# Optimization experiments

Measured on AMD Instinct MI355X. Metric: run time of the kernel, lower is better.

The kernel has to match this reference:

```python
import jax, jax.numpy as jnp
import numpy as np

N_NODES = 100000
N_EDGES = 1600000
D_IN = 128
D_OUT = 128
K_HOPS = 2


def gcn_norm(edge_index, num_nodes):
    # Add self-loops (weight 1), compute symmetric normalization
    # norm_e = deg^{-1/2}[src] * deg^{-1/2}[dst], deg over destination index.
    loop = jnp.arange(num_nodes, dtype=edge_index.dtype)
    src = jnp.concatenate([edge_index[0], loop])
    dst = jnp.concatenate([edge_index[1], loop])
    w = jnp.ones(src.shape[0], dtype=jnp.float32)
    deg = jax.ops.segment_sum(w, dst, num_segments=num_nodes)
    dinv = jnp.where(deg > 0, jax.lax.rsqrt(deg), 0.0)
    norm = dinv[src] * dinv[dst]
    return src, dst, norm


def setup_inputs() -> dict:
    key = jax.random.key(0)
    k1, k2, k3, k4 = jax.random.split(key, 4)
    x = jax.random.normal(k1, (N_NODES, D_IN), dtype=jnp.float32)
    edge_index = jax.random.randint(k2, (2, N_EDGES), 0, N_NODES, dtype=jnp.int64)
    # SGConv linear params (Glorot-ish scale)
    W = jax.random.normal(k3, (D_IN, D_OUT), dtype=jnp.float32) / np.sqrt(D_IN)
    b = jnp.zeros((D_OUT,), dtype=jnp.float32)
    return {"x": x, "edge_index": edge_index, "W": W, "b": b}


def reference(x, edge_index, W, b):
    n = x.shape[0]
    src, dst, norm = gcn_norm(edge_index, n)
    h = x
    for _ in range(K_HOPS):
        # gather source features, scale by edge norm, scatter-add to destinations
        h = jax.ops.segment_sum(h[src] * norm[:, None], dst, num_segments=n)
    return h @ W + b
```

## Files before the change

kernel.cpp:

```cpp
#include <hip/hip_runtime.h>
#include <hip/hip_bf16.h>


#define DFEAT 128
#define ELLW 64
#define ABLK 4096
#define CAP 4608
#define NBUCKMAX 512

typedef __attribute__((ext_vector_type(8))) short short8;
typedef __attribute__((ext_vector_type(4))) float f32x4;
typedef __attribute__((ext_vector_type(4))) unsigned int u32x4;

__device__ __forceinline__ float bf2f(unsigned short u) {
    union { unsigned int i; float f; } t;
    t.i = ((unsigned int)u) << 16;
    return t.f;
}

__device__ __forceinline__ unsigned short f2bf(float f) {
    union { float f; unsigned int i; } t;
    t.f = f;
    unsigned int lsb = (t.i >> 16) & 1u;
    t.i += 0x7fffu + lsb;
    return (unsigned short)(t.i >> 16);
}

__device__ __forceinline__ void accum8(float* acc, uint4 u, float w) {
    acc[0] += bf2f((unsigned short)(u.x & 0xffffu)) * w;
    acc[1] += bf2f((unsigned short)(u.x >> 16)) * w;
    acc[2] += bf2f((unsigned short)(u.y & 0xffffu)) * w;
    acc[3] += bf2f((unsigned short)(u.y >> 16)) * w;
    acc[4] += bf2f((unsigned short)(u.z & 0xffffu)) * w;
    acc[5] += bf2f((unsigned short)(u.z >> 16)) * w;
    acc[6] += bf2f((unsigned short)(u.w & 0xffffu)) * w;
    acc[7] += bf2f((unsigned short)(u.w >> 16)) * w;
}

__global__ void k_detect(const unsigned short* __restrict__ xs,
                         const int* __restrict__ ei, int* __restrict__ flags,
                         int* __restrict__ bucketCnt) {
    __shared__ int s_f32, s_oddnz;
    if (threadIdx.x == 0) { s_f32 = 0; s_oddnz = 0; }
    for (int t = threadIdx.x; t < NBUCKMAX; t += 256) bucketCnt[t] = 0;
    __syncthreads();
    int bad = 0;
    for (int i = threadIdx.x; i < 16384; i += 256) {
        unsigned int e = (xs[i] >> 7) & 0xFFu;
        if (e >= 0xC0u) bad = 1;
    }
    if (bad) atomicOr(&s_f32, 1);
    int oddnz = 0;
    for (int i = threadIdx.x; i < 4096; i += 256) {
        if (ei[2 * i + 1] != 0) oddnz = 1;
    }
    if (oddnz) atomicOr(&s_oddnz, 1);
    __syncthreads();
    if (threadIdx.x == 0) {
        flags[0] = s_f32;
        flags[1] = s_oddnz ? 0 : 1;
    }
}

__global__ void k_prepB(const void* __restrict__ Wraw, const int* __restrict__ flags,
                        unsigned short* __restrict__ Bf) {
    int t = blockIdx.x * 256 + threadIdx.x;
    if (t >= 2048) return;
    int lane = t & 63;
    int chunk = (t >> 6) & 3;
    int ntile = t >> 8;
    int ncol = ntile * 16 + (lane & 15);
    int k0 = chunk * 32 + (lane >> 4) * 8;
    int isf = flags[0];
    const float* Wf = (const float*)Wraw;
    const unsigned short* Wb = (const unsigned short*)Wraw;
    unsigned short* o = Bf + (size_t)t * 8;
#pragma unroll
    for (int j = 0; j < 8; j++) {
        int idx = (k0 + j) * DFEAT + ncol;
        o[j] = isf ? f2bf(Wf[idx]) : Wb[idx];
    }
}

__global__ __launch_bounds__(256) void k_bucketA(const int* __restrict__ ei, int E, int n,
                                                 const int* __restrict__ flags,
                                                 int* __restrict__ bucketCnt,
                                                 unsigned int* __restrict__ buck) {
    __shared__ int hist[NBUCKMAX];
    __shared__ int base[NBUCKMAX];
    for (int t = threadIdx.x; t < NBUCKMAX; t += 256) hist[t] = 0;
    __syncthreads();
    int e0 = blockIdx.x * ABLK;
    int e1 = min(E, e0 + ABLK);
    int i64 = flags[1];
    for (int e = e0 + (int)threadIdx.x; e < e1; e += 256) {
        int d = i64 ? ei[2 * (E + e)] : ei[E + e];
        atomicAdd(&hist[d >> 8], 1);
    }
    __syncthreads();
    for (int t = threadIdx.x; t < NBUCKMAX; t += 256) {
        int c = hist[t];
        base[t] = c ? atomicAdd(bucketCnt + t, c) : 0;
        hist[t] = 0;
    }
    __syncthreads();
    for (int e = e0 + (int)threadIdx.x; e < e1; e += 256) {
        int d = i64 ? ei[2 * (E + e)] : ei[E + e];
        int s = i64 ? ei[2 * e] : ei[e];
        int b = d >> 8;
        int pos = base[b] + atomicAdd(&hist[b], 1);
        if (pos < CAP)
            buck[(size_t)b * CAP + pos] = (unsigned int)s | ((unsigned int)(d & 255) << 17);
    }
}

__global__ __launch_bounds__(256) void k_bucketB(const unsigned int* __restrict__ buck,
                                                 const int* __restrict__ bucketCnt, int n,
                                                 int* __restrict__ cnt,
                                                 int* __restrict__ ell) {
    __shared__ int lcnt[256];
    int b = blockIdx.x;
    lcnt[threadIdx.x] = 0;
    __syncthreads();
    int m = min(bucketCnt[b], CAP);
    int node0 = b << 8;
    const unsigned int* bp = buck + (size_t)b * CAP;
    for (int i = threadIdx.x; i < m; i += 256) {
        unsigned int w = __builtin_nontemporal_load(bp + i);
        int s = (int)(w & 0x1FFFFu);
        int dl = (int)(w >> 17);
        int pos = atomicAdd(&lcnt[dl], 1);
        if (pos < ELLW) ell[(size_t)(node0 + dl) * ELLW + pos] = s;
    }
    __syncthreads();
    int node = node0 + (int)threadIdx.x;
    if (node < n) cnt[node] = lcnt[threadIdx.x];
}

__global__ __launch_bounds__(256) void k_gemm0(const void* __restrict__ xraw,
                                               const unsigned short* __restrict__ Bf,
                                               const int* __restrict__ flags,
                                               unsigned short* __restrict__ h0, int n) {
    __shared__ unsigned short thi[16 * 136];
    __shared__ unsigned short tlo[16 * 136];
    int wave = threadIdx.x >> 6;
    int lane = threadIdx.x & 63;
    int g = lane >> 4, c = lane & 15;
    int trow = wave * 4 + g;
    int node = blockIdx.x * 16 + trow;
    int isf = flags[0];

    uint4 ohi = {0, 0, 0, 0}, olo = {0, 0, 0, 0};
    if (node < n) {
        if (isf) {
            const float* xf = (const float*)xraw;
            f32x4 v0 = __builtin_nontemporal_load((const f32x4*)(xf + (size_t)node * DFEAT + c * 8));
            f32x4 v1 = __builtin_nontemporal_load((const f32x4*)(xf + (size_t)node * DFEAT + c * 8 + 4));
            float vv[8] = {v0[0], v0[1], v0[2], v0[3], v1[0], v1[1], v1[2], v1[3]};
            unsigned short h[8], l[8];
#pragma unroll
            for (int j = 0; j < 8; j++) {
                h[j] = f2bf(vv[j]);
                l[j] = f2bf(vv[j] - bf2f(h[j]));
            }
            ohi.x = (unsigned int)h[0] | ((unsigned int)h[1] << 16);
            ohi.y = (unsigned int)h[2] | ((unsigned int)h[3] << 16);
            ohi.z = (unsigned int)h[4] | ((unsigned int)h[5] << 16);
            ohi.w = (unsigned int)h[6] | ((unsigned int)h[7] << 16);
            olo.x = (unsigned int)l[0] | ((unsigned int)l[1] << 16);
            olo.y = (unsigned int)l[2] | ((unsigned int)l[3] << 16);
            olo.z = (unsigned int)l[4] | ((unsigned int)l[5] << 16);
            olo.w = (unsigned int)l[6] | ((unsigned int)l[7] << 16);
        } else {
            u32x4 u = __builtin_nontemporal_load(
                (const u32x4*)((const unsigned short*)xraw + (size_t)node * DFEAT + c * 8));
            ohi.x = u[0]; ohi.y = u[1]; ohi.z = u[2]; ohi.w = u[3];
        }
    }
    *(uint4*)(thi + trow * 136 + c * 8) = ohi;
    *(uint4*)(tlo + trow * 136 + c * 8) = olo;
    __syncthreads();

    int m = c, quad = g;
    f32x4 acc2[2];
    acc2[0] = (f32x4){0.f, 0.f, 0.f, 0.f};
    acc2[1] = (f32x4){0.f, 0.f, 0.f, 0.f};
#pragma unroll
    for (int c2 = 0; c2 < 4; c2++) {
        short8 ah = *(const short8*)(thi + m * 136 + c2 * 32 + quad * 8);
        short8 al = *(const short8*)(tlo + m * 136 + c2 * 32 + quad * 8);
#pragma unroll
        for (int t = 0; t < 2; t++) {
            int nt = wave * 2 + t;
            short8 bfr = *(const short8*)(Bf + ((size_t)(nt * 4 + c2) * 64 + lane) * 8);
            acc2[t] = __builtin_amdgcn_mfma_f32_16x16x32_bf16(ah, bfr, acc2[t], 0, 0, 0);
            acc2[t] = __builtin_amdgcn_mfma_f32_16x16x32_bf16(al, bfr, acc2[t], 0, 0, 0);
        }
    }

#pragma unroll
    for (int t = 0; t < 2; t++) {
        int col = (wave * 2 + t) * 16 + m;
#pragma unroll
        for (int r2 = 0; r2 < 4; r2++) {
            int grow = blockIdx.x * 16 + quad * 4 + r2;
            if (grow < n)
                __builtin_nontemporal_store(f2bf(acc2[t][r2]), h0 + (size_t)grow * DFEAT + col);
        }
    }
}

__device__ __forceinline__ void hop_accum(const unsigned short* __restrict__ fb,
                                          const int* __restrict__ ell,
                                          const int* __restrict__ cnt,
                                          int node, int lane, float* acc) {
    int g = lane >> 4, c = lane & 15;
    int deg = min(cnt[node], ELLW);
    const int* row = ell + (size_t)node * ELLW;
    float wd = rsqrtf((float)(cnt[node] + 1));
#pragma unroll
    for (int j = 0; j < 8; j++) acc[j] = 0.f;

    if (g == 0) {
        uint4 u = *(const uint4*)(fb + (size_t)node * DFEAT + c * 8);
        accum8(acc, u, wd * wd);
    }
    int last = deg - 1;
    for (int base = 0; base < deg; base += 16) {
        int k0 = base + g, k1 = k0 + 4, k2 = k0 + 8, k3 = k0 + 12;
        int s0 = __builtin_nontemporal_load(row + min(k0, last));
        int s1 = __builtin_nontemporal_load(row + min(k1, last));
        int s2 = __builtin_nontemporal_load(row + min(k2, last));
        int s3 = __builtin_nontemporal_load(row + min(k3, last));
        uint4 u0 = *(const uint4*)(fb + (size_t)s0 * DFEAT + c * 8);
        uint4 u1 = *(const uint4*)(fb + (size_t)s1 * DFEAT + c * 8);
        uint4 u2 = *(const uint4*)(fb + (size_t)s2 * DFEAT + c * 8);
        uint4 u3 = *(const uint4*)(fb + (size_t)s3 * DFEAT + c * 8);
        float w0 = (k0 < deg) ? rsqrtf((float)(cnt[s0] + 1)) * wd : 0.f;
        float w1 = (k1 < deg) ? rsqrtf((float)(cnt[s1] + 1)) * wd : 0.f;
        float w2 = (k2 < deg) ? rsqrtf((float)(cnt[s2] + 1)) * wd : 0.f;
        float w3 = (k3 < deg) ? rsqrtf((float)(cnt[s3] + 1)) * wd : 0.f;
        accum8(acc, u0, w0);
        accum8(acc, u1, w1);
        accum8(acc, u2, w2);
        accum8(acc, u3, w3);
    }
#pragma unroll
    for (int j = 0; j < 8; j++) {
        acc[j] += __shfl_xor(acc[j], 16);
        acc[j] += __shfl_xor(acc[j], 32);
    }
}

__global__ __launch_bounds__(256) void k_hop(const unsigned short* __restrict__ src,
                                             const int* __restrict__ ell,
                                             const int* __restrict__ cnt,
                                             unsigned short* __restrict__ outb, int n) {
    int node = blockIdx.x * 4 + (threadIdx.x >> 6);
    if (node >= n) return;
    int lane = threadIdx.x & 63;
    int g = lane >> 4, c = lane & 15;
    float acc[8];
    hop_accum(src, ell, cnt, node, lane, acc);
    if (g == 0) {
        uint4 o;
        o.x = (unsigned int)f2bf(acc[0]) | ((unsigned int)f2bf(acc[1]) << 16);
        o.y = (unsigned int)f2bf(acc[2]) | ((unsigned int)f2bf(acc[3]) << 16);
        o.z = (unsigned int)f2bf(acc[4]) | ((unsigned int)f2bf(acc[5]) << 16);
        o.w = (unsigned int)f2bf(acc[6]) | ((unsigned int)f2bf(acc[7]) << 16);
        *(uint4*)(outb + (size_t)node * DFEAT + c * 8) = o;
    }
}

__global__ __launch_bounds__(256) void k_hop2_out(const unsigned short* __restrict__ src,
                                                  const int* __restrict__ ell,
                                                  const int* __restrict__ cnt,
                                                  const void* __restrict__ braw,
                                                  const int* __restrict__ flags,
                                                  void* __restrict__ outraw, int n) {
    int node = blockIdx.x * 4 + (threadIdx.x >> 6);
    if (node >= n) return;
    int lane = threadIdx.x & 63;
    int g = lane >> 4, c = lane & 15;
    float acc[8];
    hop_accum(src, ell, cnt, node, lane, acc);
    if (g == 0) {
        int isf = flags[0];
        const float* bf32 = (const float*)braw;
        const unsigned short* bb16 = (const unsigned short*)braw;
#pragma unroll
        for (int j = 0; j < 8; j++)
            acc[j] += isf ? bf32[c * 8 + j] : bf2f(bb16[c * 8 + j]);
        if (isf) {
            float* outf = (float*)outraw;
            *(float4*)(outf + (size_t)node * DFEAT + c * 8) =
                (float4){acc[0], acc[1], acc[2], acc[3]};
            *(float4*)(outf + (size_t)node * DFEAT + c * 8 + 4) =
                (float4){acc[4], acc[5], acc[6], acc[7]};
        } else {
            unsigned short* outb = (unsigned short*)outraw;
            uint4 o;
            o.x = (unsigned int)f2bf(acc[0]) | ((unsigned int)f2bf(acc[1]) << 16);
            o.y = (unsigned int)f2bf(acc[2]) | ((unsigned int)f2bf(acc[3]) << 16);
            o.z = (unsigned int)f2bf(acc[4]) | ((unsigned int)f2bf(acc[5]) << 16);
            o.w = (unsigned int)f2bf(acc[6]) | ((unsigned int)f2bf(acc[7]) << 16);
            *(uint4*)(outb + (size_t)node * DFEAT + c * 8) = o;
        }
    }
}

extern "C" void kernel_launch(void* const* d_in, const int* in_sizes, int n_in,
                              void* d_out, int out_size, void* d_ws, size_t ws_size,
                              hipStream_t stream) {
    const void* x = d_in[0];
    const int* ei = (const int*)d_in[1];
    const void* W = d_in[2];
    const void* b = d_in[3];

    const int n = in_sizes[0] / DFEAT;
    const int E = in_sizes[1] / 2;

    int* ell = (int*)d_ws;
    unsigned short* h1 = (unsigned short*)(ell + (size_t)n * ELLW);
    int* cnt = (int*)(h1 + (size_t)n * DFEAT);
    int* flags = cnt + n;
    int* bucketCnt = flags + 4;
    unsigned short* Bf = (unsigned short*)(bucketCnt + NBUCKMAX);
    unsigned short* h0 = (unsigned short*)d_out;
    unsigned int* buck = (unsigned int*)((char*)d_out + (size_t)out_size
                                         - (size_t)NBUCKMAX * CAP * 4);

    k_detect<<<1, 256, 0, stream>>>((const unsigned short*)x, ei, flags, bucketCnt);

    k_prepB<<<8, 256, 0, stream>>>(W, flags, Bf);

    int nbuck = (n + 255) >> 8;
    int ablocks = (E + ABLK - 1) / ABLK;
    k_bucketA<<<ablocks, 256, 0, stream>>>(ei, E, n, flags, bucketCnt, buck);
    k_bucketB<<<nbuck, 256, 0, stream>>>(buck, bucketCnt, n, cnt, ell);

    k_gemm0<<<(n + 15) / 16, 256, 0, stream>>>(x, Bf, flags, h0, n);

    k_hop<<<(n + 3) / 4, 256, 0, stream>>>(h0, ell, cnt, h1, n);

    k_hop2_out<<<(n + 3) / 4, 256, 0, stream>>>(h1, ell, cnt, b, flags, d_out, n);
}
```

Measured before the change: 350.7 us.

## Fold GCN degree normalization into node features, drop per-edge weights

Factors the symmetric norm so node features are pre-scaled by deg^-1/2 (in the GEMM epilogue and between hops), letting the hop loops do plain unweighted sums with no per-edge cnt gathers or rsqrt. ELL rows are padded with self-indices to multiples of 16, and a correction weight on the self term makes the padding cancel, so the gather loop needs no bounds clamps. The bucketing kernel caches destination indices in shared memory and staggers global atomics, and detection now runs across 8 blocks after a memset. The change adds extra per-node scaling steps and bf16 rounding of the pre-scaled values, which may shift accuracy slightly.

```diff
diff --git a/kernel.cpp b/kernel.cpp
--- a/kernel.cpp
+++ b/kernel.cpp
@@ -11,6 +11,7 @@
 typedef __attribute__((ext_vector_type(8))) short short8;
 typedef __attribute__((ext_vector_type(4))) float f32x4;
 typedef __attribute__((ext_vector_type(4))) unsigned int u32x4;
+typedef __attribute__((ext_vector_type(4))) int i32x4;
 
 __device__ __forceinline__ float bf2f(unsigned short u) {
     union { unsigned int i; float f; } t;
@@ -37,29 +38,32 @@
     acc[7] += bf2f((unsigned short)(u.w >> 16)) * w;
 }
 
+__device__ __forceinline__ void add8(float* acc, uint4 u) {
+    union { unsigned int i; float f; } a;
+    a.i = u.x << 16;          acc[0] += a.f;
+    a.i = u.x & 0xffff0000u;  acc[1] += a.f;
+    a.i = u.y << 16;          acc[2] += a.f;
+    a.i = u.y & 0xffff0000u;  acc[3] += a.f;
+    a.i = u.z << 16;          acc[4] += a.f;
+    a.i = u.z & 0xffff0000u;  acc[5] += a.f;
+    a.i = u.w << 16;          acc[6] += a.f;
+    a.i = u.w & 0xffff0000u;  acc[7] += a.f;
+}
+
 __global__ void k_detect(const unsigned short* __restrict__ xs,
-                         const int* __restrict__ ei, int* __restrict__ flags,
-                         int* __restrict__ bucketCnt) {
-    __shared__ int s_f32, s_oddnz;
-    if (threadIdx.x == 0) { s_f32 = 0; s_oddnz = 0; }
-    for (int t = threadIdx.x; t < NBUCKMAX; t += 256) bucketCnt[t] = 0;
-    __syncthreads();
+                         const int* __restrict__ ei, int* __restrict__ flags) {
+    int t = blockIdx.x * 256 + (int)threadIdx.x;
     int bad = 0;
-    for (int i = threadIdx.x; i < 16384; i += 256) {
+    for (int i = t; i < 16384; i += 2048) {
         unsigned int e = (xs[i] >> 7) & 0xFFu;
         if (e >= 0xC0u) bad = 1;
     }
-    if (bad) atomicOr(&s_f32, 1);
+    if (__any(bad) && (threadIdx.x & 63) == 0) atomicOr(flags, 1);
     int oddnz = 0;
-    for (int i = threadIdx.x; i < 4096; i += 256) {
+    for (int i = t; i < 4096; i += 2048) {
         if (ei[2 * i + 1] != 0) oddnz = 1;
     }
-    if (oddnz) atomicOr(&s_oddnz, 1);
-    __syncthreads();
-    if (threadIdx.x == 0) {
-        flags[0] = s_f32;
-        flags[1] = s_oddnz ? 0 : 1;
-    }
+    if (__any(oddnz) && (threadIdx.x & 63) == 0) atomicOr(flags + 1, 1);
 }
 
 __global__ void k_prepB(const void* __restrict__ Wraw, const int* __restrict__ flags,
@@ -86,29 +90,35 @@
                                                  const int* __restrict__ flags,
                                                  int* __restrict__ bucketCnt,
                                                  unsigned int* __restrict__ buck) {
+    __shared__ int sd[ABLK];
     __shared__ int hist[NBUCKMAX];
-    __shared__ int base[NBUCKMAX];
+    __shared__ int base_[NBUCKMAX];
     for (int t = threadIdx.x; t < NBUCKMAX; t += 256) hist[t] = 0;
     __syncthreads();
     int e0 = blockIdx.x * ABLK;
     int e1 = min(E, e0 + ABLK);
-    int i64 = flags[1];
+    int i64 = (flags[1] == 0);
     for (int e = e0 + (int)threadIdx.x; e < e1; e += 256) {
-        int d = i64 ? ei[2 * (E + e)] : ei[E + e];
+        int d = i64 ? __builtin_nontemporal_load(ei + 2 * (E + e))
+                    : __builtin_nontemporal_load(ei + E + e);
+        sd[e - e0] = d;
         atomicAdd(&hist[d >> 8], 1);
     }
     __syncthreads();
-    for (int t = threadIdx.x; t < NBUCKMAX; t += 256) {
-        int c = hist[t];
-        base[t] = c ? atomicAdd(bucketCnt + t, c) : 0;
+#pragma unroll
+    for (int r = 0; r < 2; r++) {
+        int t = ((int)threadIdx.x + r * 256 + (int)blockIdx.x * 61) & (NBUCKMAX - 1);
+        int cc = hist[t];
+        base_[t] = cc ? atomicAdd(bucketCnt + t, cc) : 0;
         hist[t] = 0;
     }
     __syncthreads();
     for (int e = e0 + (int)threadIdx.x; e < e1; e += 256) {
-        int d = i64 ? ei[2 * (E + e)] : ei[E + e];
-        int s = i64 ? ei[2 * e] : ei[e];
+        int d = sd[e - e0];
+        int s = i64 ? __builtin_nontemporal_load(ei + 2 * e)
+                    : __builtin_nontemporal_load(ei + e);
         int b = d >> 8;
-        int pos = base[b] + atomicAdd(&hist[b], 1);
+        int pos = base_[b] + atomicAdd(&hist[b], 1);
         if (pos < CAP)
             buck[(size_t)b * CAP + pos] = (unsigned int)s | ((unsigned int)(d & 255) << 17);
     }
@@ -134,13 +144,21 @@
     }
     __syncthreads();
     int node = node0 + (int)threadIdx.x;
-    if (node < n) cnt[node] = lcnt[threadIdx.x];
+    if (node < n) {
+        int c = lcnt[threadIdx.x];
+        cnt[node] = c;
+        int st = min(c, ELLW);
+        int slots = min((c + 16) & ~15, ELLW);
+        int* rowp = ell + (size_t)node * ELLW;
+        for (int p = st; p < slots; p++) rowp[p] = node;
+    }
 }
 
 __global__ __launch_bounds__(256) void k_gemm0(const void* __restrict__ xraw,
                                                const unsigned short* __restrict__ Bf,
                                                const int* __restrict__ flags,
-                                               unsigned short* __restrict__ h0, int n) {
+                                               const int* __restrict__ cnt,
+                                               unsigned short* __restrict__ g0, int n) {
     __shared__ unsigned short thi[16 * 136];
     __shared__ unsigned short tlo[16 * 136];
     int wave = threadIdx.x >> 6;
@@ -198,6 +216,12 @@
         }
     }
 
+    float sc[4];
+#pragma unroll
+    for (int r2 = 0; r2 < 4; r2++) {
+        int grow = blockIdx.x * 16 + quad * 4 + r2;
+        sc[r2] = (grow < n) ? rsqrtf((float)(cnt[grow] + 1)) : 0.f;
+    }
 #pragma unroll
     for (int t = 0; t < 2; t++) {
         int col = (wave * 2 + t) * 16 + m;
@@ -205,45 +229,36 @@
         for (int r2 = 0; r2 < 4; r2++) {
             int grow = blockIdx.x * 16 + quad * 4 + r2;
             if (grow < n)
-                __builtin_nontemporal_store(f2bf(acc2[t][r2]), h0 + (size_t)grow * DFEAT + col);
+                __builtin_nontemporal_store(f2bf(acc2[t][r2] * sc[r2]),
+                                            g0 + (size_t)grow * DFEAT + col);
         }
     }
 }
 
 __device__ __forceinline__ void hop_accum(const unsigned short* __restrict__ fb,
                                           const int* __restrict__ ell,
-                                          const int* __restrict__ cnt,
-                                          int node, int lane, float* acc) {
+                                          int node, int cn, int lane, float* acc) {
     int g = lane >> 4, c = lane & 15;
-    int deg = min(cnt[node], ELLW);
+    int slots = min((cn + 16) & ~15, ELLW);
     const int* row = ell + (size_t)node * ELLW;
-    float wd = rsqrtf((float)(cnt[node] + 1));
 #pragma unroll
     for (int j = 0; j < 8; j++) acc[j] = 0.f;
 
-    if (g == 0) {
+    for (int base = 0; base < slots; base += 16) {
+        i32x4 s4 = __builtin_nontemporal_load((const i32x4*)(row + base) + g);
+        uint4 u0 = *(const uint4*)(fb + (size_t)s4[0] * DFEAT + c * 8);
+        uint4 u1 = *(const uint4*)(fb + (size_t)s4[1] * DFEAT + c * 8);
+        uint4 u2 = *(const uint4*)(fb + (size_t)s4[2] * DFEAT + c * 8);
+        uint4 u3 = *(const uint4*)(fb + (size_t)s4[3] * DFEAT + c * 8);
+        add8(acc, u0);
+        add8(acc, u1);
+        add8(acc, u2);
+        add8(acc, u3);
+    }
+    float corrw = (cn < ELLW) ? (float)(cn + 1 - slots) : 1.0f;
+    if (g == 0 && corrw != 0.0f) {
         uint4 u = *(const uint4*)(fb + (size_t)node * DFEAT + c * 8);
-        accum8(acc, u, wd * wd);
-    }
-    int last = deg - 1;
-    for (int base = 0; base < deg; base += 16) {
-        int k0 = base + g, k1 = k0 + 4, k2 = k0 + 8, k3 = k0 + 12;
-        int s0 = __builtin_nontemporal_load(row + min(k0, last));
-        int s1 = __builtin_nontemporal_load(row + min(k1, last));
-        int s2 = __builtin_nontemporal_load(row + min(k2, last));
-        int s3 = __builtin_nontemporal_load(row + min(k3, last));
-        uint4 u0 = *(const uint4*)(fb + (size_t)s0 * DFEAT + c * 8);
-        uint4 u1 = *(const uint4*)(fb + (size_t)s1 * DFEAT + c * 8);
-        uint4 u2 = *(const uint4*)(fb + (size_t)s2 * DFEAT + c * 8);
-        uint4 u3 = *(const uint4*)(fb + (size_t)s3 * DFEAT + c * 8);
-        float w0 = (k0 < deg) ? rsqrtf((float)(cnt[s0] + 1)) * wd : 0.f;
-        float w1 = (k1 < deg) ? rsqrtf((float)(cnt[s1] + 1)) * wd : 0.f;
-        float w2 = (k2 < deg) ? rsqrtf((float)(cnt[s2] + 1)) * wd : 0.f;
-        float w3 = (k3 < deg) ? rsqrtf((float)(cnt[s3] + 1)) * wd : 0.f;
-        accum8(acc, u0, w0);
-        accum8(acc, u1, w1);
-        accum8(acc, u2, w2);
-        accum8(acc, u3, w3);
+        accum8(acc, u, corrw);
     }
 #pragma unroll
     for (int j = 0; j < 8; j++) {
@@ -259,15 +274,17 @@
     int node = blockIdx.x * 4 + (threadIdx.x >> 6);
     if (node >= n) return;
     int lane = threadIdx.x & 63;
-    int g = lane >> 4, c = lane & 15;
+    int cn = cnt[node];
     float acc[8];
-    hop_accum(src, ell, cnt, node, lane, acc);
-    if (g == 0) {
+    hop_accum(src, ell, node, cn, lane, acc);
+    if ((lane >> 4) == 0) {
+        int c = lane & 15;
+        float sc = 1.0f / (float)(cn + 1);
         uint4 o;
-        o.x = (unsigned int)f2bf(acc[0]) | ((unsigned int)f2bf(acc[1]) << 16);
-        o.y = (unsigned int)f2bf(acc[2]) | ((unsigned int)f2bf(acc[3]) << 16);
-        o.z = (unsigned int)f2bf(acc[4]) | ((unsigned int)f2bf(acc[5]) << 16);
-        o.w = (unsigned int)f2bf(acc[6]) | ((unsigned int)f2bf(acc[7]) << 16);
+        o.x = (unsigned int)f2bf(acc[0] * sc) | ((unsigned int)f2bf(acc[1] * sc) << 16);
+        o.y = (unsigned int)f2bf(acc[2] * sc) | ((unsigned int)f2bf(acc[3] * sc) << 16);
+        o.z = (unsigned int)f2bf(acc[4] * sc) | ((unsigned int)f2bf(acc[5] * sc) << 16);
+        o.w = (unsigned int)f2bf(acc[6] * sc) | ((unsigned int)f2bf(acc[7] * sc) << 16);
         *(uint4*)(outb + (size_t)node * DFEAT + c * 8) = o;
     }
 }
@@ -281,16 +298,20 @@
     int node = blockIdx.x * 4 + (threadIdx.x >> 6);
     if (node >= n) return;
     int lane = threadIdx.x & 63;
-    int g = lane >> 4, c = lane & 15;
+    int cn = cnt[node];
     float acc[8];
-    hop_accum(src, ell, cnt, node, lane, acc);
-    if (g == 0) {
+    hop_accum(src, ell, node, cn, lane, acc);
+    if ((lane >> 4) == 0) {
+        int c = lane & 15;
+        float sc = rsqrtf((float)(cn + 1));
         int isf = flags[0];
         const float* bf32 = (const float*)braw;
         const unsigned short* bb16 = (const unsigned short*)braw;
 #pragma unroll
-        for (int j = 0; j < 8; j++)
-            acc[j] += isf ? bf32[c * 8 + j] : bf2f(bb16[c * 8 + j]);
+        for (int j = 0; j < 8; j++) {
+            float bias = isf ? bf32[c * 8 + j] : bf2f(bb16[c * 8 + j]);
+            acc[j] = acc[j] * sc + bias;
+        }
         if (isf) {
             float* outf = (float*)outraw;
             *(float4*)(outf + (size_t)node * DFEAT + c * 8) =
@@ -321,16 +342,18 @@
     const int E = in_sizes[1] / 2;
 
     int* ell = (int*)d_ws;
-    unsigned short* h1 = (unsigned short*)(ell + (size_t)n * ELLW);
-    int* cnt = (int*)(h1 + (size_t)n * DFEAT);
+    unsigned short* g1 = (unsigned short*)(ell + (size_t)n * ELLW);
+    int* cnt = (int*)(g1 + (size_t)n * DFEAT);
     int* flags = cnt + n;
     int* bucketCnt = flags + 4;
     unsigned short* Bf = (unsigned short*)(bucketCnt + NBUCKMAX);
-    unsigned short* h0 = (unsigned short*)d_out;
+    unsigned short* g0 = (unsigned short*)d_out;
     unsigned int* buck = (unsigned int*)((char*)d_out + (size_t)out_size
                                          - (size_t)NBUCKMAX * CAP * 4);
 
-    k_detect<<<1, 256, 0, stream>>>((const unsigned short*)x, ei, flags, bucketCnt);
+    (void)hipMemsetAsync(flags, 0, (4 + NBUCKMAX) * sizeof(int), stream);
+
+    k_detect<<<8, 256, 0, stream>>>((const unsigned short*)x, ei, flags);
 
     k_prepB<<<8, 256, 0, stream>>>(W, flags, Bf);
 
@@ -339,9 +362,9 @@
     k_bucketA<<<ablocks, 256, 0, stream>>>(ei, E, n, flags, bucketCnt, buck);
     k_bucketB<<<nbuck, 256, 0, stream>>>(buck, bucketCnt, n, cnt, ell);
 
-    k_gemm0<<<(n + 15) / 16, 256, 0, stream>>>(x, Bf, flags, h0, n);
-
-    k_hop<<<(n + 3) / 4, 256, 0, stream>>>(h0, ell, cnt, h1, n);
-
-    k_hop2_out<<<(n + 3) / 4, 256, 0, stream>>>(h1, ell, cnt, b, flags, d_out, n);
-}
+    k_gemm0<<<(n + 15) / 16, 256, 0, stream>>>(x, Bf, flags, cnt, g0, n);
+
+    k_hop<<<(n + 3) / 4, 256, 0, stream>>>(g0, ell, cnt, g1, n);
+
+    k_hop2_out<<<(n + 3) / 4, 256, 0, stream>>>(g1, ell, cnt, b, flags, d_out, n);
+}
```

Result: faster. 316.4 us (-9.8%).
